# Kernel tuning notes

Hardware: AMD Instinct MI355X
Metric: run time of the kernel (lower is better)

## Reference

```python
import jax, jax.numpy as jnp
import numpy as np

H = 16       # num query heads
KV = 4       # num kv heads
D = 64       # head_dim
EPS = 1e-6


def setup_inputs() -> dict:
    key = jax.random.key(0)
    ks = jax.random.split(key, 12)
    B, N, E = 2, 2048, 1024
    s = 0.02
    return {
        "x": jax.random.normal(ks[0], (B, N, E), jnp.float32),
        "sin": jax.random.normal(ks[1], (N, D), jnp.float32),
        "cos": jax.random.normal(ks[2], (N, D), jnp.float32),
        "wq_w": jax.random.normal(ks[3], (E, E), jnp.float32) * s,
        "wq_b": jax.random.normal(ks[4], (E,), jnp.float32) * s,
        "wk_w": jax.random.normal(ks[5], (KV * D, E), jnp.float32) * s,
        "wk_b": jax.random.normal(ks[6], (KV * D,), jnp.float32) * s,
        "wv_w": jax.random.normal(ks[7], (KV * D, E), jnp.float32) * s,
        "wv_b": jax.random.normal(ks[8], (KV * D,), jnp.float32) * s,
        "qn_w": jnp.ones((D,), jnp.float32),
        "kn_w": jnp.ones((D,), jnp.float32),
        "proj_w": jax.random.normal(ks[9], (E, E), jnp.float32) * s,
        "proj_b": jax.random.normal(ks[10], (E,), jnp.float32) * s,
    }


def _rmsnorm(t, w):
    # t: [..., D]
    var = jnp.mean(t * t, axis=-1, keepdims=True)
    return t * jax.lax.rsqrt(var + EPS) * w


def _rope(t, sin, cos):
    # t: [B,h,N,D]; sin/cos: [N,D] broadcast
    x1, x2 = jnp.split(t, 2, axis=-1)
    rotated = jnp.concatenate([-x2, x1], axis=-1)
    return t * cos + rotated * sin


def reference(x, sin, cos, wq_w, wq_b, wk_w, wk_b, wv_w, wv_b,
              qn_w, kn_w, proj_w, proj_b):
    B, N, E = x.shape
    q = (x @ wq_w.T + wq_b).reshape(B, N, H, D).transpose(0, 2, 1, 3)   # [B,H,N,D]
    k = (x @ wk_w.T + wk_b).reshape(B, N, KV, D).transpose(0, 2, 1, 3)  # [B,KV,N,D]
    v = (x @ wv_w.T + wv_b).reshape(B, N, KV, D).transpose(0, 2, 1, 3)
    q = _rmsnorm(q, qn_w)
    k = _rmsnorm(k, kn_w)
    # GQA: repeat kv heads to match query heads (repeat_interleave on head dim)
    factor = H // KV
    k = jnp.repeat(k, factor, axis=1)  # [B,H,N,D]
    v = jnp.repeat(v, factor, axis=1)
    # RoPE (n_extra = 0 since sin covers full sequence)
    q = _rope(q, sin, cos)
    k = _rope(k, sin, cos)
    # scaled dot-product attention
    scale = 1.0 / np.sqrt(D).astype(np.float32)
    scores = jnp.einsum("bhqd,bhkd->bhqk", q, k) * scale
    attn = jax.nn.softmax(scores, axis=-1)
    out = jnp.einsum("bhqk,bhkd->bhqd", attn, v)      # [B,H,N,D]
    out = out.transpose(0, 2, 1, 3).reshape(B, N, E)  # [B,N,E]
    return out @ proj_w.T + proj_b
```

## Files before the change

### kernel.cpp

```cpp
#include <hip/hip_runtime.h>
#include <hip/hip_bf16.h>
#include <math.h>


#define N_SEQ 2048
#define EMB   1024
#define NH    16
#define NKV   4
#define HD    64
#define BATCH 2
#define M_TOT 4096
#define QKV_N 1536

typedef __attribute__((ext_vector_type(8)))  short short8;
typedef __attribute__((ext_vector_type(4)))  float f32x4;
typedef __attribute__((ext_vector_type(16))) float f32x16;

__device__ __forceinline__ ushort f2bf(float f) {
    union { __hip_bfloat16 h; ushort u; } cv;
    cv.h = __float2bfloat16(f);
    return cv.u;
}
__device__ __forceinline__ float bf2f(ushort u) {
    union { __hip_bfloat16 h; ushort u; } cv;
    cv.u = u;
    return __bfloat162float(cv.h);
}
__device__ __forceinline__ uint pack2bf(float a, float b) {
    union { __hip_bfloat162 h; uint u; } cv;
    cv.h = __float22bfloat162_rn(float2{a, b});
    return cv.u;
}

__device__ __forceinline__ void g2lds16(const ushort* g, ushort* l) {
    __builtin_amdgcn_global_load_lds(
        (const __attribute__((address_space(1))) unsigned int*)g,
        (__attribute__((address_space(3))) unsigned int*)l, 16, 0, 0);
}

__device__ __forceinline__ void stage3(const ushort* Ap, const ushort* Wp,
                                       int K, ushort* AsW, ushort* BsW, int kk)
{
    g2lds16(Ap + kk, AsW);
    g2lds16(Ap + (size_t)64 * K + kk, AsW + 2048);
    g2lds16(Wp + kk, BsW);
}

__device__ __forceinline__ void mfma_phase(const ushort* __restrict__ Asb,
                                           const ushort* __restrict__ Bsb,
                                           int wm, int l16, int quad,
                                           f32x4 (&acc)[2][4])
{
    short8 aF[2], bF[4];
#pragma unroll
    for (int i = 0; i < 2; ++i)
        aF[i] = *(const short8*)&Asb[(wm + i * 16 + l16) * 32 + quad * 8];
#pragma unroll
    for (int j = 0; j < 4; ++j)
        bF[j] = *(const short8*)&Bsb[(j * 16 + l16) * 32 + quad * 8];
    __builtin_amdgcn_s_setprio(1);
#pragma unroll
    for (int i = 0; i < 2; ++i)
#pragma unroll
        for (int j = 0; j < 4; ++j)
            acc[i][j] = __builtin_amdgcn_mfma_f32_16x16x32_bf16(
                aF[i], bF[j], acc[i][j], 0, 0, 0);
    __builtin_amdgcn_s_setprio(0);
}

__device__ __forceinline__ void cvt4(const float* __restrict__ s,
                                     ushort* __restrict__ d, long g, long gd) {
    const float4 v = ((const float4*)s)[g];
    ushort4 o;
    o.x = f2bf(v.x); o.y = f2bf(v.y); o.z = f2bf(v.z); o.w = f2bf(v.w);
    ((ushort4*)d)[gd] = o;
}

__global__ __launch_bounds__(256) void prep_kernel(
    const float* __restrict__ x,  const float* __restrict__ wq,
    const float* __restrict__ wk, const float* __restrict__ wv,
    const float* __restrict__ wp, const float* __restrict__ bq,
    const float* __restrict__ bk, const float* __restrict__ bv,
    ushort* __restrict__ xb, ushort* __restrict__ Wqkv,
    ushort* __restrict__ Wproj, float* __restrict__ bqkv)
{
    const long i = (long)blockIdx.x * 256 + threadIdx.x;
    if (i < 1048576) {
        cvt4(x, xb, i, i);
    } else if (i < 1310720) {
        const long g = i - 1048576;
        cvt4(wq, Wqkv, g, g);
    } else if (i < 1376256) {
        const long g = i - 1310720;
        cvt4(wk, Wqkv, g, 262144 + g);
    } else if (i < 1441792) {
        const long g = i - 1376256;
        cvt4(wv, Wqkv, g, 327680 + g);
    } else if (i < 1703936) {
        const long g = i - 1441792;
        cvt4(wp, Wproj, g, g);
    } else if (i < 1704320) {
        const long j = i - 1703936;
        float4 v;
        if (j < 256)      v = ((const float4*)bq)[j];
        else if (j < 320) v = ((const float4*)bk)[j - 256];
        else              v = ((const float4*)bv)[j - 320];
        ((float4*)bqkv)[j] = v;
    }
}

__global__ __launch_bounds__(256) void gemm_qkv_fused(
    const ushort* __restrict__ A, const ushort* __restrict__ W,
    const float* __restrict__ bias,
    const float* __restrict__ qn_w, const float* __restrict__ kn_w,
    const float* __restrict__ sinp, const float* __restrict__ cosp,
    ushort* __restrict__ Qb, ushort* __restrict__ Kf,
    ushort* __restrict__ Vf)
{
    __shared__ ushort SMEM[12288];
    ushort* As0 = SMEM;
    ushort* Bs0 = SMEM + 4096;
    ushort* As1 = SMEM + 6144;
    ushort* Bs1 = SMEM + 10240;

    const int tid = threadIdx.x;
    const int m0 = blockIdx.y * 128, n0 = blockIdx.x * 64;
    const int w = tid >> 6, lane = tid & 63;
    const int quad = lane >> 4, l16 = lane & 15;
    const int wm = w * 32;
    const int K = EMB;

    f32x4 acc[2][4] = {};

    float bb[4];
#pragma unroll
    for (int j = 0; j < 4; ++j) bb[j] = bias[n0 + j * 16 + l16];

    const int r0 = tid >> 2;
    const int c8 = (tid & 3) * 8;
    const ushort* Ap = A + (size_t)(m0 + r0) * K + c8;
    const ushort* Wp = W + (size_t)(n0 + r0) * K + c8;
    ushort* As0W = As0 + w * 512;
    ushort* Bs0W = Bs0 + w * 512;
    ushort* As1W = As1 + w * 512;
    ushort* Bs1W = Bs1 + w * 512;

    stage3(Ap, Wp, K, As0W, Bs0W, 0);
    for (int k0 = 0; k0 < K; k0 += 64) {
        __syncthreads();
        stage3(Ap, Wp, K, As1W, Bs1W, k0 + 32);
        mfma_phase(As0, Bs0, wm, l16, quad, acc);
        __syncthreads();
        if (k0 + 64 < K) stage3(Ap, Wp, K, As0W, Bs0W, k0 + 64);
        mfma_phase(As1, Bs1, wm, l16, quad, acc);
    }

    if (n0 < 1280) {
        const bool isQ = (n0 < 1024);
        const float* nw = isQ ? qn_w : kn_w;
        const float oscale = isQ ? 0.125f : 1.0f;
        float nwv[4];
#pragma unroll
        for (int j = 0; j < 4; ++j) nwv[j] = nw[j * 16 + l16];

#pragma unroll
        for (int i = 0; i < 2; ++i) {
#pragma unroll
            for (int r = 0; r < 4; ++r) {
                const int m = m0 + wm + i * 16 + quad * 4 + r;
                const int n = m & (N_SEQ - 1);
                const int bI = m >> 11;

                float v4[4];
                float ssum = 0.0f;
#pragma unroll
                for (int j = 0; j < 4; ++j) {
                    v4[j] = acc[i][j][r] + bb[j];
                    ssum += v4[j] * v4[j];
                }
                ssum += __shfl_xor(ssum, 1, 64);
                ssum += __shfl_xor(ssum, 2, 64);
                ssum += __shfl_xor(ssum, 4, 64);
                ssum += __shfl_xor(ssum, 8, 64);
                const float rinv = rsqrtf(ssum * (1.0f / 64.0f) + 1e-6f);

                float tn[4], val[4];
#pragma unroll
                for (int j = 0; j < 4; ++j) tn[j] = v4[j] * rinv * nwv[j];
#pragma unroll
                for (int j = 0; j < 4; ++j) {
                    const int d = j * 16 + l16;
                    const float rot = (j < 2) ? -tn[j + 2] : tn[j - 2];
                    val[j] = (tn[j] * cosp[n * HD + d] + rot * sinp[n * HD + d]) * oscale;
                }

                if (isQ) {
                    const size_t qrow =
                        ((size_t)((bI << 4) + (n0 >> 6)) * N_SEQ + n) * HD;
#pragma unroll
                    for (int j = 0; j < 4; ++j)
                        Qb[qrow + j * 16 + l16] = f2bf(val[j]);
                } else {
                    const int kvh = (n0 >> 6) - 16;
                    const int kt = n >> 6, rr = n & 63;
                    const int ss2 = rr >> 5, l32k = rr & 31;
                    const size_t kb =
                        ((size_t)(bI * NKV + kvh) * 32 + kt) * 4096 + l32k * 16 + l16;
#pragma unroll
                    for (int j = 0; j < 4; ++j)
                        Kf[kb + (ss2 * 4 + j) * 512] = f2bf(val[j]);
                }
            }
        }
    } else {
        const int kvv = (n0 - 1280) >> 6;
        const int bI = m0 >> 11;
        const int kt0 = (m0 & (N_SEQ - 1)) >> 6;
        ushort* L = SMEM;

        const int c = tid >> 5;
        const int l32v = tid & 31;
        const int row0 = (c >> 2) * 32 + ((c >> 1) & 1) * 16;
        const int dcol = (c & 1) * 32 + l32v;

#pragma unroll
        for (int h = 0; h < 2; ++h) {
            __syncthreads();
            if ((w >> 1) == h) {
                const int kl0 = wm - h * 64;
#pragma unroll
                for (int i = 0; i < 2; ++i)
#pragma unroll
                    for (int r = 0; r < 4; ++r) {
                        const int kl = kl0 + i * 16 + quad * 4 + r;
#pragma unroll
                        for (int j = 0; j < 4; ++j)
                            L[kl * 68 + j * 16 + l16] = f2bf(acc[i][j][r] + bb[j]);
                    }
            }
            __syncthreads();
            short8 o0, o1;
#pragma unroll
            for (int e = 0; e < 8; ++e) o0[e] = (short)L[(row0 + e) * 68 + dcol];
#pragma unroll
            for (int e = 0; e < 8; ++e) o1[e] = (short)L[(row0 + 8 + e) * 68 + dcol];
            const size_t vb = ((size_t)(bI * NKV + kvv) * 32 + kt0 + h) * 4096
                              + c * 512 + l32v * 16;
            *(short8*)&Vf[vb] = o0;
            *(short8*)&Vf[vb + 8] = o1;
        }
    }
}

template <bool BF16OUT>
__global__ __launch_bounds__(256) void gemm_mfma_kernel(
    const ushort* __restrict__ A, const ushort* __restrict__ W,
    const float* __restrict__ bias, void* __restrict__ Cout,
    int K, int ldc)
{
    __shared__ ushort SMEM[12288];
    ushort* As0 = SMEM;
    ushort* Bs0 = SMEM + 4096;
    ushort* As1 = SMEM + 6144;
    ushort* Bs1 = SMEM + 10240;

    const int tid = threadIdx.x;
    const int m0 = blockIdx.y * 128, n0 = blockIdx.x * 64;
    const int w = tid >> 6, lane = tid & 63;
    const int quad = lane >> 4, l16 = lane & 15;
    const int wm = w * 32;

    f32x4 acc[2][4] = {};

    float bb[4];
#pragma unroll
    for (int j = 0; j < 4; ++j) bb[j] = bias[n0 + j * 16 + l16];

    const int r0 = tid >> 2;
    const int c8 = (tid & 3) * 8;
    const ushort* Ap = A + (size_t)(m0 + r0) * K + c8;
    const ushort* Wp = W + (size_t)(n0 + r0) * K + c8;
    ushort* As0W = As0 + w * 512;
    ushort* Bs0W = Bs0 + w * 512;
    ushort* As1W = As1 + w * 512;
    ushort* Bs1W = Bs1 + w * 512;

    stage3(Ap, Wp, K, As0W, Bs0W, 0);
    for (int k0 = 0; k0 < K; k0 += 64) {
        __syncthreads();
        stage3(Ap, Wp, K, As1W, Bs1W, k0 + 32);
        mfma_phase(As0, Bs0, wm, l16, quad, acc);
        __syncthreads();
        if (k0 + 64 < K) stage3(Ap, Wp, K, As0W, Bs0W, k0 + 64);
        mfma_phase(As1, Bs1, wm, l16, quad, acc);
    }

#pragma unroll
    for (int i = 0; i < 2; ++i) {
        const int rowb = m0 + wm + i * 16 + quad * 4;
#pragma unroll
        for (int j = 0; j < 4; ++j) {
            const int col = n0 + j * 16 + l16;
#pragma unroll
            for (int r = 0; r < 4; ++r) {
                const float vv = acc[i][j][r] + bb[j];
                if (BF16OUT)
                    ((ushort*)Cout)[(size_t)(rowb + r) * ldc + col] = f2bf(vv);
                else
                    ((float*)Cout)[(size_t)(rowb + r) * ldc + col] = vv;
            }
        }
    }
}

__global__ __launch_bounds__(256, 4) void flash_mfma32_kernel(
    const ushort* __restrict__ Qb, const ushort* __restrict__ Kf,
    const ushort* __restrict__ Vf, ushort* __restrict__ Ob)
{
    __shared__ float fsm[4352];

    const int qt = blockIdx.x;
    const int bh = blockIdx.y;
    const int b = bh >> 4, h = bh & 15;
    const int kvh = h >> 2;
    const int tid = threadIdx.x;
    const int w = tid >> 6, lane = tid & 63;
    const int l32 = lane & 31, l5 = lane >> 5;
    const int qg = w & 1;
    const int kh = w >> 1;

    const ushort* Qg = Qb + ((size_t)bh * N_SEQ + qt * 64 + qg * 32) * HD;
    const size_t kvbase = (size_t)(b * NKV + kvh) * (32 * 4096);
    const ushort* Kp = Kf + kvbase;
    const ushort* Vp = Vf + kvbase;
    const int loff = l32 * 16 + l5 * 8;

    short8 qF[4];
#pragma unroll
    for (int c = 0; c < 4; ++c)
        qF[c] = *(const short8*)&Qg[(size_t)l32 * HD + c * 16 + l5 * 8];

    f32x16 Oa[2] = {};
    float mrow = -3.0e38f, lrow = 0.0f;

    for (int i = 0; i < 16; ++i) {
        const int kt = kh * 16 + i;
        const ushort* Kt = Kp + kt * 4096;
        const ushort* Vt = Vp + kt * 4096;

        short8 kT[2][4];
#pragma unroll
        for (int s = 0; s < 2; ++s)
#pragma unroll
            for (int c = 0; c < 4; ++c)
                kT[s][c] = *(const short8*)&Kt[(s * 4 + c) * 512 + loff];
        short8 vT[2][2][2];
#pragma unroll
        for (int s = 0; s < 2; ++s)
#pragma unroll
            for (int t = 0; t < 2; ++t)
#pragma unroll
                for (int d2 = 0; d2 < 2; ++d2)
                    vT[s][t][d2] = *(const short8*)&Vt[((s * 2 + t) * 2 + d2) * 512 + loff];

        f32x16 Sv[2] = {};
#pragma unroll
        for (int s = 0; s < 2; ++s)
#pragma unroll
            for (int c = 0; c < 4; ++c)
                Sv[s] = __builtin_amdgcn_mfma_f32_32x32x16_bf16(kT[s][c], qF[c], Sv[s], 0, 0, 0);

        float mx = -3.0e38f;
#pragma unroll
        for (int s = 0; s < 2; ++s)
#pragma unroll
            for (int r = 0; r < 16; ++r) mx = fmaxf(mx, Sv[s][r]);
        mx = fmaxf(mx, __shfl_xor(mx, 32, 64));
        const float mnew = fmaxf(mrow, mx);
        const float alpha = __expf(mrow - mnew);
        mrow = mnew;
        float rs = 0.0f;
#pragma unroll
        for (int s = 0; s < 2; ++s)
#pragma unroll
            for (int r = 0; r < 16; ++r) {
                Sv[s][r] = __expf(Sv[s][r] - mnew);
                rs += Sv[s][r];
            }
        rs += __shfl_xor(rs, 32, 64);
        lrow = lrow * alpha + rs;
#pragma unroll
        for (int t = 0; t < 2; ++t)
#pragma unroll
            for (int r = 0; r < 16; ++r) Oa[t][r] *= alpha;

        uint P2[2][8];
#pragma unroll
        for (int s = 0; s < 2; ++s)
#pragma unroll
            for (int g = 0; g < 4; ++g)
#pragma unroll
                for (int hh = 0; hh < 2; ++hh)
                    P2[s][g * 2 + hh] =
                        pack2bf(Sv[s][4 * g + 2 * hh], Sv[s][4 * g + 2 * hh + 1]);

#pragma unroll
        for (int s = 0; s < 2; ++s)
#pragma unroll
            for (int t = 0; t < 2; ++t) {
                const uint snd0 = l5 ? P2[s][4 * t + 0] : P2[s][4 * t + 2];
                const uint snd1 = l5 ? P2[s][4 * t + 1] : P2[s][4 * t + 3];
                const uint kp0  = l5 ? P2[s][4 * t + 2] : P2[s][4 * t + 0];
                const uint kp1  = l5 ? P2[s][4 * t + 3] : P2[s][4 * t + 1];
                const uint rcv0 = __shfl_xor(snd0, 32, 64);
                const uint rcv1 = __shfl_xor(snd1, 32, 64);
                union { uint u[4]; short8 s8; } pb;
                pb.u[0] = l5 ? rcv0 : kp0;
                pb.u[1] = l5 ? rcv1 : kp1;
                pb.u[2] = l5 ? kp0 : rcv0;
                pb.u[3] = l5 ? kp1 : rcv1;
#pragma unroll
                for (int d2 = 0; d2 < 2; ++d2)
                    Oa[d2] = __builtin_amdgcn_mfma_f32_32x32x16_bf16(
                        vT[s][t][d2], pb.s8, Oa[d2], 0, 0, 0);
            }
    }

    float* buf = fsm + qg * 2176;
    if (kh == 1) {
#pragma unroll
        for (int d2 = 0; d2 < 2; ++d2)
#pragma unroll
            for (int r = 0; r < 16; ++r)
                buf[(d2 * 16 + r) * 64 + lane] = Oa[d2][r];
        buf[2048 + lane] = mrow;
        buf[2112 + lane] = lrow;
    }
    __syncthreads();

    if (kh == 0) {
        const float mb = buf[2048 + lane];
        const float lb = buf[2112 + lane];
        const float M = fmaxf(mrow, mb);
        const float ea = __expf(mrow - M), eb = __expf(mb - M);
        lrow = lrow * ea + lb * eb;
#pragma unroll
        for (int d2 = 0; d2 < 2; ++d2)
#pragma unroll
            for (int r = 0; r < 16; ++r)
                Oa[d2][r] = Oa[d2][r] * ea + buf[(d2 * 16 + r) * 64 + lane] * eb;
    }
    __syncthreads();

    ushort* Os = (ushort*)fsm;
    if (kh == 0) {
        const float inv = 1.0f / lrow;
#pragma unroll
        for (int d2 = 0; d2 < 2; ++d2)
#pragma unroll
            for (int r = 0; r < 16; ++r) {
                const int d = d2 * 32 + (r & 3) + 8 * (r >> 2) + 4 * l5;
                Os[(qg * 32 + l32) * 68 + d] = f2bf(Oa[d2][r] * inv);
            }
    }
    __syncthreads();

    const int row = tid >> 2, cc = (tid & 3) * 16;
#pragma unroll
    for (int i = 0; i < 2; ++i) {
        const short8 v = *(const short8*)&Os[row * 68 + cc + i * 8];
        *(short8*)&Ob[((size_t)b * N_SEQ + qt * 64 + row) * EMB + h * HD + cc + i * 8] = v;
    }
}

extern "C" void kernel_launch(void* const* d_in, const int* in_sizes, int n_in,
                              void* d_out, int out_size, void* d_ws, size_t ws_size,
                              hipStream_t stream)
{
    const float* x      = (const float*)d_in[0];
    const float* sinp   = (const float*)d_in[1];
    const float* cosp   = (const float*)d_in[2];
    const float* wq_w   = (const float*)d_in[3];
    const float* wq_b   = (const float*)d_in[4];
    const float* wk_w   = (const float*)d_in[5];
    const float* wk_b   = (const float*)d_in[6];
    const float* wv_w   = (const float*)d_in[7];
    const float* wv_b   = (const float*)d_in[8];
    const float* qn_w   = (const float*)d_in[9];
    const float* kn_w   = (const float*)d_in[10];
    const float* proj_w = (const float*)d_in[11];
    const float* proj_b = (const float*)d_in[12];
    float* out = (float*)d_out;

    ushort* Tq    = (ushort*)d_ws;
    ushort* xb    = Tq + 6291456;
    ushort* Wqkv  = xb + 4194304;
    ushort* Wproj = Wqkv + 1572864;
    float*  bqkv  = (float*)(Wproj + 1048576);
    ushort* Qb    = (ushort*)(bqkv + 1536);
    ushort* Kf    = Qb + 4194304;
    ushort* Vf    = Kf + 1048576;

    prep_kernel<<<6658, 256, 0, stream>>>(x, wq_w, wk_w, wv_w, proj_w,
                                          wq_b, wk_b, wv_b,
                                          xb, Wqkv, Wproj, bqkv);

    gemm_qkv_fused<<<dim3(QKV_N / 64, M_TOT / 128), 256, 0, stream>>>(
        xb, Wqkv, bqkv, qn_w, kn_w, sinp, cosp, Qb, Kf, Vf);

    flash_mfma32_kernel<<<dim3(32, 32), 256, 0, stream>>>(Qb, Kf, Vf, xb);

    gemm_mfma_kernel<false><<<dim3(EMB / 64, M_TOT / 128), 256, 0, stream>>>(
        xb, Wproj, proj_b, out, EMB, EMB);
}
```

Baseline: 199.2 us.

## Use triple-buffered LDS pipeline with explicit vmcnt waits in GEMM k-loops

Replaces the double-buffered k-loop in both the fused QKV GEMM and the generic GEMM with a three-stage LDS ring. Explicit s_waitcnt vmcnt and s_barrier calls let two tiles stay in flight while the current one is computed. The goal is to hide global-to-LDS load latency better than waiting on each stage with __syncthreads. It raises LDS use per block from 24KB to 36KB, which may reduce occupancy, and the hand-written vmcnt counts must match the loads in flight exactly.

```diff
diff --git a/kernel.cpp b/kernel.cpp
--- a/kernel.cpp
+++ b/kernel.cpp
@@ -16,6 +16,9 @@
 typedef __attribute__((ext_vector_type(4)))  float f32x4;
 typedef __attribute__((ext_vector_type(16))) float f32x16;
 
+#define VMCNT(n) asm volatile("s_waitcnt vmcnt(" #n ")" ::: "memory")
+#define BARM()   asm volatile("s_barrier" ::: "memory")
+
 __device__ __forceinline__ ushort f2bf(float f) {
     union { __hip_bfloat16 h; ushort u; } cv;
     cv.h = __float2bfloat16(f);
@@ -39,18 +42,19 @@
 }
 
 __device__ __forceinline__ void stage3(const ushort* Ap, const ushort* Wp,
-                                       int K, ushort* AsW, ushort* BsW, int kk)
-{
-    g2lds16(Ap + kk, AsW);
-    g2lds16(Ap + (size_t)64 * K + kk, AsW + 2048);
-    g2lds16(Wp + kk, BsW);
-}
-
-__device__ __forceinline__ void mfma_phase(const ushort* __restrict__ Asb,
-                                           const ushort* __restrict__ Bsb,
+                                       int K, ushort* buf, int w, int kk)
+{
+    g2lds16(Ap + kk, buf + w * 512);
+    g2lds16(Ap + (size_t)64 * K + kk, buf + 2048 + w * 512);
+    g2lds16(Wp + kk, buf + 4096 + w * 512);
+}
+
+__device__ __forceinline__ void mfma_phase(const ushort* __restrict__ buf,
                                            int wm, int l16, int quad,
                                            f32x4 (&acc)[2][4])
 {
+    const ushort* Asb = buf;
+    const ushort* Bsb = buf + 4096;
     short8 aF[2], bF[4];
 #pragma unroll
     for (int i = 0; i < 2; ++i)
@@ -66,6 +70,45 @@
             acc[i][j] = __builtin_amdgcn_mfma_f32_16x16x32_bf16(
                 aF[i], bF[j], acc[i][j], 0, 0, 0);
     __builtin_amdgcn_s_setprio(0);
+}
+
+__device__ __forceinline__ void kloop_pipe3(const ushort* Ap, const ushort* Wp,
+                                            int K, ushort* b0, ushort* b1,
+                                            ushort* b2, int w, int wm,
+                                            int l16, int quad,
+                                            f32x4 (&acc)[2][4])
+{
+    stage3(Ap, Wp, K, b0, w, 0);
+    stage3(Ap, Wp, K, b1, w, 32);
+    stage3(Ap, Wp, K, b2, w, 64);
+    for (int k0 = 0; k0 + 160 < K; k0 += 96) {
+        VMCNT(6); BARM();
+        mfma_phase(b0, wm, l16, quad, acc);
+        BARM();
+        stage3(Ap, Wp, K, b0, w, k0 + 96);
+        VMCNT(6); BARM();
+        mfma_phase(b1, wm, l16, quad, acc);
+        BARM();
+        stage3(Ap, Wp, K, b1, w, k0 + 128);
+        VMCNT(6); BARM();
+        mfma_phase(b2, wm, l16, quad, acc);
+        BARM();
+        stage3(Ap, Wp, K, b2, w, k0 + 160);
+    }
+    VMCNT(6); BARM();
+    mfma_phase(b0, wm, l16, quad, acc);
+    BARM();
+    stage3(Ap, Wp, K, b0, w, K - 64);
+    VMCNT(6); BARM();
+    mfma_phase(b1, wm, l16, quad, acc);
+    BARM();
+    stage3(Ap, Wp, K, b1, w, K - 32);
+    VMCNT(6); BARM();
+    mfma_phase(b2, wm, l16, quad, acc);
+    VMCNT(3); BARM();
+    mfma_phase(b0, wm, l16, quad, acc);
+    VMCNT(0); BARM();
+    mfma_phase(b1, wm, l16, quad, acc);
 }
 
 __device__ __forceinline__ void cvt4(const float* __restrict__ s,
@@ -117,11 +160,10 @@
     ushort* __restrict__ Qb, ushort* __restrict__ Kf,
     ushort* __restrict__ Vf)
 {
-    __shared__ ushort SMEM[12288];
-    ushort* As0 = SMEM;
-    ushort* Bs0 = SMEM + 4096;
-    ushort* As1 = SMEM + 6144;
-    ushort* Bs1 = SMEM + 10240;
+    __shared__ ushort SMEM[18432];
+    ushort* b0 = SMEM;
+    ushort* b1 = SMEM + 6144;
+    ushort* b2 = SMEM + 12288;
 
     const int tid = threadIdx.x;
     const int m0 = blockIdx.y * 128, n0 = blockIdx.x * 64;
@@ -140,20 +182,8 @@
     const int c8 = (tid & 3) * 8;
     const ushort* Ap = A + (size_t)(m0 + r0) * K + c8;
     const ushort* Wp = W + (size_t)(n0 + r0) * K + c8;
-    ushort* As0W = As0 + w * 512;
-    ushort* Bs0W = Bs0 + w * 512;
-    ushort* As1W = As1 + w * 512;
-    ushort* Bs1W = Bs1 + w * 512;
-
-    stage3(Ap, Wp, K, As0W, Bs0W, 0);
-    for (int k0 = 0; k0 < K; k0 += 64) {
-        __syncthreads();
-        stage3(Ap, Wp, K, As1W, Bs1W, k0 + 32);
-        mfma_phase(As0, Bs0, wm, l16, quad, acc);
-        __syncthreads();
-        if (k0 + 64 < K) stage3(Ap, Wp, K, As0W, Bs0W, k0 + 64);
-        mfma_phase(As1, Bs1, wm, l16, quad, acc);
-    }
+
+    kloop_pipe3(Ap, Wp, K, b0, b1, b2, w, wm, l16, quad, acc);
 
     if (n0 < 1280) {
         const bool isQ = (n0 < 1024);
@@ -258,11 +288,10 @@
     const float* __restrict__ bias, void* __restrict__ Cout,
     int K, int ldc)
 {
-    __shared__ ushort SMEM[12288];
-    ushort* As0 = SMEM;
-    ushort* Bs0 = SMEM + 4096;
-    ushort* As1 = SMEM + 6144;
-    ushort* Bs1 = SMEM + 10240;
+    __shared__ ushort SMEM[18432];
+    ushort* b0 = SMEM;
+    ushort* b1 = SMEM + 6144;
+    ushort* b2 = SMEM + 12288;
 
     const int tid = threadIdx.x;
     const int m0 = blockIdx.y * 128, n0 = blockIdx.x * 64;
@@ -280,20 +309,8 @@
     const int c8 = (tid & 3) * 8;
     const ushort* Ap = A + (size_t)(m0 + r0) * K + c8;
     const ushort* Wp = W + (size_t)(n0 + r0) * K + c8;
-    ushort* As0W = As0 + w * 512;
-    ushort* Bs0W = Bs0 + w * 512;
-    ushort* As1W = As1 + w * 512;
-    ushort* Bs1W = Bs1 + w * 512;
-
-    stage3(Ap, Wp, K, As0W, Bs0W, 0);
-    for (int k0 = 0; k0 < K; k0 += 64) {
-        __syncthreads();
-        stage3(Ap, Wp, K, As1W, Bs1W, k0 + 32);
-        mfma_phase(As0, Bs0, wm, l16, quad, acc);
-        __syncthreads();
-        if (k0 + 64 < K) stage3(Ap, Wp, K, As0W, Bs0W, k0 + 64);
-        mfma_phase(As1, Bs1, wm, l16, quad, acc);
-    }
+
+    kloop_pipe3(Ap, Wp, K, b0, b1, b2, w, wm, l16, quad, acc);
 
 #pragma unroll
     for (int i = 0; i < 2; ++i) {
```

Result: no change. 197.1 us (-1.1%).

## Fuse fp32-to-bf16 conversion into GEMM loads and drop prep kernel

Applied to the files above, without the earlier changes.

Removes the separate prep kernel that converted x and all weights to bf16. The QKV and projection GEMMs now read fp32 directly through registers, pack to bf16, and write to LDS in a register-staged double-buffer pipeline instead of global_load_lds. A block-index swizzle is also added for L2 locality. The cost is that each GEMM tile re-reads and re-converts fp32 data (x is read 24 times across N tiles), global traffic for the A operand doubles, and register pressure rises.

```diff
diff --git a/kernel.cpp b/kernel.cpp
--- a/kernel.cpp
+++ b/kernel.cpp
@@ -31,26 +31,19 @@
     cv.h = __float22bfloat162_rn(float2{a, b});
     return cv.u;
 }
-
-__device__ __forceinline__ void g2lds16(const ushort* g, ushort* l) {
-    __builtin_amdgcn_global_load_lds(
-        (const __attribute__((address_space(1))) unsigned int*)g,
-        (__attribute__((address_space(3))) unsigned int*)l, 16, 0, 0);
-}
-
-__device__ __forceinline__ void stage3(const ushort* Ap, const ushort* Wp,
-                                       int K, ushort* AsW, ushort* BsW, int kk)
-{
-    g2lds16(Ap + kk, AsW);
-    g2lds16(Ap + (size_t)64 * K + kk, AsW + 2048);
-    g2lds16(Wp + kk, BsW);
-}
-
-__device__ __forceinline__ void mfma_phase(const ushort* __restrict__ Asb,
-                                           const ushort* __restrict__ Bsb,
+__device__ __forceinline__ short8 pack8(float4 a, float4 b) {
+    union { uint u[4]; short8 s; } o;
+    o.u[0] = pack2bf(a.x, a.y); o.u[1] = pack2bf(a.z, a.w);
+    o.u[2] = pack2bf(b.x, b.y); o.u[3] = pack2bf(b.z, b.w);
+    return o.s;
+}
+
+__device__ __forceinline__ void mfma_phase(const ushort* __restrict__ buf,
                                            int wm, int l16, int quad,
                                            f32x4 (&acc)[2][4])
 {
+    const ushort* Asb = buf;
+    const ushort* Bsb = buf + 4096;
     short8 aF[2], bF[4];
 #pragma unroll
     for (int i = 0; i < 2; ++i)
@@ -68,63 +61,25 @@
     __builtin_amdgcn_s_setprio(0);
 }
 
-__device__ __forceinline__ void cvt4(const float* __restrict__ s,
-                                     ushort* __restrict__ d, long g, long gd) {
-    const float4 v = ((const float4*)s)[g];
-    ushort4 o;
-    o.x = f2bf(v.x); o.y = f2bf(v.y); o.z = f2bf(v.z); o.w = f2bf(v.w);
-    ((ushort4*)d)[gd] = o;
-}
-
-__global__ __launch_bounds__(256) void prep_kernel(
-    const float* __restrict__ x,  const float* __restrict__ wq,
-    const float* __restrict__ wk, const float* __restrict__ wv,
-    const float* __restrict__ wp, const float* __restrict__ bq,
+__global__ __launch_bounds__(256) void gemm_qkv_fused(
+    const float* __restrict__ x,
+    const float* __restrict__ wq, const float* __restrict__ wk,
+    const float* __restrict__ wv, const float* __restrict__ bq,
     const float* __restrict__ bk, const float* __restrict__ bv,
-    ushort* __restrict__ xb, ushort* __restrict__ Wqkv,
-    ushort* __restrict__ Wproj, float* __restrict__ bqkv)
-{
-    const long i = (long)blockIdx.x * 256 + threadIdx.x;
-    if (i < 1048576) {
-        cvt4(x, xb, i, i);
-    } else if (i < 1310720) {
-        const long g = i - 1048576;
-        cvt4(wq, Wqkv, g, g);
-    } else if (i < 1376256) {
-        const long g = i - 1310720;
-        cvt4(wk, Wqkv, g, 262144 + g);
-    } else if (i < 1441792) {
-        const long g = i - 1376256;
-        cvt4(wv, Wqkv, g, 327680 + g);
-    } else if (i < 1703936) {
-        const long g = i - 1441792;
-        cvt4(wp, Wproj, g, g);
-    } else if (i < 1704320) {
-        const long j = i - 1703936;
-        float4 v;
-        if (j < 256)      v = ((const float4*)bq)[j];
-        else if (j < 320) v = ((const float4*)bk)[j - 256];
-        else              v = ((const float4*)bv)[j - 320];
-        ((float4*)bqkv)[j] = v;
-    }
-}
-
-__global__ __launch_bounds__(256) void gemm_qkv_fused(
-    const ushort* __restrict__ A, const ushort* __restrict__ W,
-    const float* __restrict__ bias,
     const float* __restrict__ qn_w, const float* __restrict__ kn_w,
     const float* __restrict__ sinp, const float* __restrict__ cosp,
     ushort* __restrict__ Qb, ushort* __restrict__ Kf,
     ushort* __restrict__ Vf)
 {
     __shared__ ushort SMEM[12288];
-    ushort* As0 = SMEM;
-    ushort* Bs0 = SMEM + 4096;
-    ushort* As1 = SMEM + 6144;
-    ushort* Bs1 = SMEM + 10240;
+    ushort* buf0 = SMEM;
+    ushort* buf1 = SMEM + 6144;
 
     const int tid = threadIdx.x;
-    const int m0 = blockIdx.y * 128, n0 = blockIdx.x * 64;
+    const int bid = blockIdx.x;
+    const int swz = (bid & 7) * 96 + (bid >> 3);
+    const int bx = swz % 24, by = swz / 24;
+    const int m0 = by * 128, n0 = bx * 64;
     const int w = tid >> 6, lane = tid & 63;
     const int quad = lane >> 4, l16 = lane & 15;
     const int wm = w * 32;
@@ -132,28 +87,52 @@
 
     f32x4 acc[2][4] = {};
 
+    const float* Wbase; const float* bbase;
+    if (n0 < 1024)      { Wbase = wq + (size_t)n0 * K;          bbase = bq + n0; }
+    else if (n0 < 1280) { Wbase = wk + (size_t)(n0 - 1024) * K; bbase = bk + (n0 - 1024); }
+    else                { Wbase = wv + (size_t)(n0 - 1280) * K; bbase = bv + (n0 - 1280); }
+
     float bb[4];
 #pragma unroll
-    for (int j = 0; j < 4; ++j) bb[j] = bias[n0 + j * 16 + l16];
+    for (int j = 0; j < 4; ++j) bb[j] = bbase[j * 16 + l16];
 
     const int r0 = tid >> 2;
     const int c8 = (tid & 3) * 8;
-    const ushort* Ap = A + (size_t)(m0 + r0) * K + c8;
-    const ushort* Wp = W + (size_t)(n0 + r0) * K + c8;
-    ushort* As0W = As0 + w * 512;
-    ushort* Bs0W = Bs0 + w * 512;
-    ushort* As1W = As1 + w * 512;
-    ushort* Bs1W = Bs1 + w * 512;
-
-    stage3(Ap, Wp, K, As0W, Bs0W, 0);
+    const float* Ap = x + (size_t)(m0 + r0) * K + c8;
+    const float* Wp = Wbase + (size_t)r0 * K + c8;
+
+    float4 a00A, a01A, a10A, a11A, w0A, w1A;
+    float4 a00B, a01B, a10B, a11B, w0B, w1B;
+
+#define LOADQ(S, kk)                                            \
+    a00##S = *(const float4*)(Ap + (kk));                       \
+    a01##S = *(const float4*)(Ap + (kk) + 4);                   \
+    a10##S = *(const float4*)(Ap + (size_t)64 * K + (kk));      \
+    a11##S = *(const float4*)(Ap + (size_t)64 * K + (kk) + 4);  \
+    w0##S  = *(const float4*)(Wp + (kk));                       \
+    w1##S  = *(const float4*)(Wp + (kk) + 4)
+
+#define WRITEQ(S, dst)                                                   \
+    *(short8*)&(dst)[r0 * 32 + c8]          = pack8(a00##S, a01##S);     \
+    *(short8*)&(dst)[(r0 + 64) * 32 + c8]   = pack8(a10##S, a11##S);     \
+    *(short8*)&(dst)[4096 + r0 * 32 + c8]   = pack8(w0##S, w1##S)
+
+    LOADQ(A, 0);
+    WRITEQ(A, buf0);
+    LOADQ(A, 32);
+    __syncthreads();
     for (int k0 = 0; k0 < K; k0 += 64) {
+        if (k0 + 64 < K) { LOADQ(B, k0 + 64); }
+        mfma_phase(buf0, wm, l16, quad, acc);
+        WRITEQ(A, buf1);
         __syncthreads();
-        stage3(Ap, Wp, K, As1W, Bs1W, k0 + 32);
-        mfma_phase(As0, Bs0, wm, l16, quad, acc);
+        if (k0 + 96 < K) { LOADQ(A, k0 + 96); }
+        mfma_phase(buf1, wm, l16, quad, acc);
+        if (k0 + 64 < K) { WRITEQ(B, buf0); }
         __syncthreads();
-        if (k0 + 64 < K) stage3(Ap, Wp, K, As0W, Bs0W, k0 + 64);
-        mfma_phase(As1, Bs1, wm, l16, quad, acc);
-    }
+    }
+#undef LOADQ
+#undef WRITEQ
 
     if (n0 < 1280) {
         const bool isQ = (n0 < 1024);
@@ -252,20 +231,20 @@
     }
 }
 
-template <bool BF16OUT>
-__global__ __launch_bounds__(256) void gemm_mfma_kernel(
-    const ushort* __restrict__ A, const ushort* __restrict__ W,
-    const float* __restrict__ bias, void* __restrict__ Cout,
-    int K, int ldc)
+__global__ __launch_bounds__(256) void gemm_proj(
+    const ushort* __restrict__ A, const float* __restrict__ W,
+    const float* __restrict__ bias, float* __restrict__ Cout)
 {
     __shared__ ushort SMEM[12288];
-    ushort* As0 = SMEM;
-    ushort* Bs0 = SMEM + 4096;
-    ushort* As1 = SMEM + 6144;
-    ushort* Bs1 = SMEM + 10240;
+    ushort* buf0 = SMEM;
+    ushort* buf1 = SMEM + 6144;
 
     const int tid = threadIdx.x;
-    const int m0 = blockIdx.y * 128, n0 = blockIdx.x * 64;
+    const int K = EMB;
+    const int bid = blockIdx.x;
+    const int swz = (bid & 7) * 64 + (bid >> 3);
+    const int bx = swz % 16, by = swz / 16;
+    const int m0 = by * 128, n0 = bx * 64;
     const int w = tid >> 6, lane = tid & 63;
     const int quad = lane >> 4, l16 = lane & 15;
     const int wm = w * 32;
@@ -279,21 +258,38 @@
     const int r0 = tid >> 2;
     const int c8 = (tid & 3) * 8;
     const ushort* Ap = A + (size_t)(m0 + r0) * K + c8;
-    const ushort* Wp = W + (size_t)(n0 + r0) * K + c8;
-    ushort* As0W = As0 + w * 512;
-    ushort* Bs0W = Bs0 + w * 512;
-    ushort* As1W = As1 + w * 512;
-    ushort* Bs1W = Bs1 + w * 512;
-
-    stage3(Ap, Wp, K, As0W, Bs0W, 0);
+    const float*  Wp = W + (size_t)(n0 + r0) * K + c8;
+
+    short8 a0A, a1A; float4 w0A, w1A;
+    short8 a0B, a1B; float4 w0B, w1B;
+
+#define LOADP(S, kk)                                            \
+    a0##S = *(const short8*)(Ap + (kk));                        \
+    a1##S = *(const short8*)(Ap + (size_t)64 * K + (kk));       \
+    w0##S = *(const float4*)(Wp + (kk));                        \
+    w1##S = *(const float4*)(Wp + (kk) + 4)
+
+#define WRITEP(S, dst)                                          \
+    *(short8*)&(dst)[r0 * 32 + c8]        = a0##S;              \
+    *(short8*)&(dst)[(r0 + 64) * 32 + c8] = a1##S;              \
+    *(short8*)&(dst)[4096 + r0 * 32 + c8] = pack8(w0##S, w1##S)
+
+    LOADP(A, 0);
+    WRITEP(A, buf0);
+    LOADP(A, 32);
+    __syncthreads();
     for (int k0 = 0; k0 < K; k0 += 64) {
+        if (k0 + 64 < K) { LOADP(B, k0 + 64); }
+        mfma_phase(buf0, wm, l16, quad, acc);
+        WRITEP(A, buf1);
         __syncthreads();
-        stage3(Ap, Wp, K, As1W, Bs1W, k0 + 32);
-        mfma_phase(As0, Bs0, wm, l16, quad, acc);
+        if (k0 + 96 < K) { LOADP(A, k0 + 96); }
+        mfma_phase(buf1, wm, l16, quad, acc);
+        if (k0 + 64 < K) { WRITEP(B, buf0); }
         __syncthreads();
-        if (k0 + 64 < K) stage3(Ap, Wp, K, As0W, Bs0W, k0 + 64);
-        mfma_phase(As1, Bs1, wm, l16, quad, acc);
-    }
+    }
+#undef LOADP
+#undef WRITEP
 
 #pragma unroll
     for (int i = 0; i < 2; ++i) {
@@ -302,13 +298,8 @@
         for (int j = 0; j < 4; ++j) {
             const int col = n0 + j * 16 + l16;
 #pragma unroll
-            for (int r = 0; r < 4; ++r) {
-                const float vv = acc[i][j][r] + bb[j];
-                if (BF16OUT)
-                    ((ushort*)Cout)[(size_t)(rowb + r) * ldc + col] = f2bf(vv);
-                else
-                    ((float*)Cout)[(size_t)(rowb + r) * ldc + col] = vv;
-            }
+            for (int r = 0; r < 4; ++r)
+                Cout[(size_t)(rowb + r) * EMB + col] = acc[i][j][r] + bb[j];
         }
     }
 }
@@ -501,15 +492,11 @@
     ushort* Kf    = Qb + 4194304;
     ushort* Vf    = Kf + 1048576;
 
-    prep_kernel<<<6658, 256, 0, stream>>>(x, wq_w, wk_w, wv_w, proj_w,
-                                          wq_b, wk_b, wv_b,
-                                          xb, Wqkv, Wproj, bqkv);
-
-    gemm_qkv_fused<<<dim3(QKV_N / 64, M_TOT / 128), 256, 0, stream>>>(
-        xb, Wqkv, bqkv, qn_w, kn_w, sinp, cosp, Qb, Kf, Vf);
+    gemm_qkv_fused<<<768, 256, 0, stream>>>(
+        x, wq_w, wk_w, wv_w, wq_b, wk_b, wv_b,
+        qn_w, kn_w, sinp, cosp, Qb, Kf, Vf);
 
     flash_mfma32_kernel<<<dim3(32, 32), 256, 0, stream>>>(Qb, Kf, Vf, xb);
 
-    gemm_mfma_kernel<false><<<dim3(EMB / 64, M_TOT / 128), 256, 0, stream>>>(
-        xb, Wproj, proj_b, out, EMB, EMB);
-}
+    gemm_proj<<<512, 256, 0, stream>>>(xb, proj_w, proj_b, out);
+}
```

After: 202.0 us. About the same (+1.4%).
